# Kernel tuning notes

Measured on AMD Instinct MI355X. Metric: run time of the kernel, lower is better.

## Reference

```python
import jax, jax.numpy as jnp
import numpy as np

EMBED_DIM = 768
NUM_HEADS = 12


def setup_inputs() -> dict:
    key = jax.random.key(0)
    ks = jax.random.split(key, 9)
    B, N, C = 16, 1024, EMBED_DIM
    std = 1.0 / np.sqrt(C)
    x = jax.random.normal(ks[0], (B, N, C), dtype=jnp.float32)
    def w(k):
        return jax.random.normal(k, (C, C), dtype=jnp.float32) * std
    def b(k):
        return jax.random.normal(k, (C,), dtype=jnp.float32) * 0.01
    return {
        "x": x,
        "Wq": w(ks[1]), "bq": b(ks[2]),
        "Wk": w(ks[3]), "bk": b(ks[4]),
        "Wv": w(ks[5]), "bv": b(ks[6]),
        "Wo": w(ks[7]), "bo": b(ks[8]),
    }


def reference(x, Wq, bq, Wk, bk, Wv, bv, Wo, bo):
    B, N, C = x.shape
    H = NUM_HEADS
    Dh = C // H
    scale = 1.0 / np.sqrt(Dh)

    q = x @ Wq + bq  # (B, N, C)
    k = x @ Wk + bk
    v = x @ Wv + bv

    # Faithful to the original: (B, N, H, Dh) -> reshape(B*H, N, Dh)
    # WITHOUT transposing, exactly as torch_mla_core does (row-major reshape).
    q2 = q.reshape(B * H, N, Dh)
    k2 = k.reshape(B * H, N, Dh)
    v2 = v.reshape(B * H, N, Dh)

    scores = jnp.einsum('gld,gmd->glm', q2, k2) * scale  # (B*H, N, N)
    attn = jax.nn.softmax(scores, axis=-1)
    ctx2 = jnp.einsum('glm,gmd->gld', attn, v2)  # (B*H, N, Dh)

    ctx = ctx2.reshape(B, H, N, Dh).transpose(0, 2, 1, 3).reshape(B, N, C)
    out = ctx @ Wo + bo
    return out
```

## Files before the change

kernel.cpp:

```cpp
#include <hip/hip_runtime.h>
#include <cstdint>
#include <cstddef>

typedef unsigned short u16;
typedef __attribute__((ext_vector_type(8))) short s8v;
typedef __attribute__((ext_vector_type(4))) float f4v;
typedef __attribute__((ext_vector_type(8))) u16 u16x8;

#define AS1 __attribute__((address_space(1)))
#define AS3 __attribute__((address_space(3)))

#define BATCH 16
#define SEQ   1024
#define EMBED 768
#define HEADS 12
#define DH    64
#define GROUPS (BATCH*HEADS)
#define MTOT  (BATCH*SEQ)

__device__ __forceinline__ u16 f2bf(float f) {
    union { float f; uint32_t u; } v; v.f = f;
    uint32_t r = v.u + 0x7fffu + ((v.u >> 16) & 1u);
    return (u16)(r >> 16);
}

__device__ __forceinline__ void gll16(const u16* g, u16* l) {
    __builtin_amdgcn_global_load_lds((AS1 void*)g, (AS3 void*)l, 16, 0, 0);
}

__global__ void k_pack_x(const float* __restrict__ x, u16* __restrict__ xb, int n) {
    int i = (blockIdx.x * 256 + threadIdx.x) * 4;
    if (i + 3 < n) {
        float4 f = *(const float4*)(x + i);
        ushort4 o;
        o.x = f2bf(f.x); o.y = f2bf(f.y); o.z = f2bf(f.z); o.w = f2bf(f.w);
        *(ushort4*)(xb + i) = o;
    }
}

__global__ void k_pack_w(const float* __restrict__ Wq, const float* __restrict__ Wk,
                         const float* __restrict__ Wv, const float* __restrict__ Wo,
                         const float* __restrict__ bq, const float* __restrict__ bk,
                         const float* __restrict__ bv,
                         u16* __restrict__ wqkvT, u16* __restrict__ woT,
                         float* __restrict__ bqkv)
{
    const int NQKV = 2304 * 768;
    const int NO = 768 * 768;
    int t = blockIdx.x * 256 + threadIdx.x;
    if (t < NQKV) {
        int n = t % 2304, k = t / 2304;
        const float* src; int nn; float sc;
        if (n < 768)       { src = Wq; nn = n;        sc = 0.125f; }
        else if (n < 1536) { src = Wk; nn = n - 768;  sc = 1.0f;   }
        else               { src = Wv; nn = n - 1536; sc = 1.0f;   }
        wqkvT[(size_t)n * 768 + k] = f2bf(src[(size_t)k * 768 + nn] * sc);
    } else if (t < NQKV + NO) {
        int t2 = t - NQKV;
        int n = t2 % 768, k = t2 / 768;
        woT[(size_t)n * 768 + k] = f2bf(Wo[(size_t)k * 768 + n]);
    } else if (t < NQKV + NO + 2304) {
        int t3 = t - NQKV - NO;
        bqkv[t3] = (t3 < 768) ? bq[t3] * 0.125f
                 : ((t3 < 1536) ? bk[t3 - 768] : bv[t3 - 1536]);
    }
}

template<int MODE>
__global__ __launch_bounds__(256) void k_gemm(
    const u16* __restrict__ A, const u16* __restrict__ BT,
    const float* __restrict__ bias,
    u16* __restrict__ oq, u16* __restrict__ okk, u16* __restrict__ ov,
    float* __restrict__ of)
{
    __shared__ __attribute__((aligned(16))) u16 As[128 * 32];
    __shared__ __attribute__((aligned(16))) u16 Bs[128 * 32];
    const int tid = threadIdx.x;
    const int m0 = blockIdx.x * 128;
    const int n0 = blockIdx.y * 128;
    const int wv = tid >> 6;
    const int ln = tid & 63;
    const int l15 = ln & 15, quad = ln >> 4;
    const int wm = (wv >> 1) * 64, wn = (wv & 1) * 64;
    const int r = tid >> 2, c8 = (tid & 3) * 8;

    const u16* gA0 = A + (size_t)(m0 + r) * 768 + c8;
    const u16* gA1 = gA0 + 64 * 768;
    const u16* gB0 = BT + (size_t)(n0 + r) * 768 + c8;
    const u16* gB1 = gB0 + 64 * 768;
    u16* lA0 = As + wv * 512;
    u16* lA1 = As + 2048 + wv * 512;
    u16* lB0 = Bs + wv * 512;
    u16* lB1 = Bs + 2048 + wv * 512;

    f4v acc[4][4] = {};

    for (int kt = 0; kt < 24; ++kt) {
        const int ko = kt * 32;
        gll16(gA0 + ko, lA0);
        gll16(gA1 + ko, lA1);
        gll16(gB0 + ko, lB0);
        gll16(gB1 + ko, lB1);
        __syncthreads();
        s8v aF[4], bF[4];
#pragma unroll
        for (int i = 0; i < 4; ++i)
            aF[i] = *(const s8v*)(As + (wm + i * 16 + l15) * 32 + quad * 8);
#pragma unroll
        for (int j = 0; j < 4; ++j)
            bF[j] = *(const s8v*)(Bs + (wn + j * 16 + l15) * 32 + quad * 8);
#pragma unroll
        for (int i = 0; i < 4; ++i)
#pragma unroll
            for (int j = 0; j < 4; ++j)
                acc[i][j] = __builtin_amdgcn_mfma_f32_16x16x32_bf16(aF[i], bF[j], acc[i][j], 0, 0, 0);
        __syncthreads();
    }

#pragma unroll
    for (int j = 0; j < 4; ++j) {
        int n = n0 + wn + j * 16 + l15;
        float bs = bias[n];
        if (MODE == 0) {
            u16* dst; int nn;
            if (n < 768)       { dst = oq;  nn = n; }
            else if (n < 1536) { dst = okk; nn = n - 768; }
            else               { dst = ov;  nn = n - 1536; }
#pragma unroll
            for (int i = 0; i < 4; ++i) {
                int mrow = m0 + wm + i * 16 + quad * 4;
#pragma unroll
                for (int rg = 0; rg < 4; ++rg)
                    dst[(size_t)(mrow + rg) * 768 + nn] = f2bf(acc[i][j][rg] + bs);
            }
        } else {
#pragma unroll
            for (int i = 0; i < 4; ++i) {
                int mrow = m0 + wm + i * 16 + quad * 4;
#pragma unroll
                for (int rg = 0; rg < 4; ++rg)
                    of[(size_t)(mrow + rg) * 768 + n] = acc[i][j][rg] + bs;
            }
        }
    }
}

__global__ void k_transpose_v(const u16* __restrict__ v, u16* __restrict__ vt) {
    __shared__ __attribute__((aligned(16))) u16 ts[64 * 72];
    int g = blockIdx.x >> 4;
    int l0 = (blockIdx.x & 15) << 6;
    const u16* vg = v + (size_t)g * 65536;
    u16* vtg = vt + (size_t)g * 65536;
    int tid = threadIdx.x;
#pragma unroll
    for (int c = tid; c < 512; c += 256) {
        int l = c >> 3, d0 = (c & 7) * 8;
        *(uint4*)(ts + l * 72 + d0) = *(const uint4*)(vg + (size_t)(l0 + l) * 64 + d0);
    }
    __syncthreads();
#pragma unroll
    for (int c = tid; c < 512; c += 256) {
        int d = c >> 3, lc = (c & 7) * 8;
        u16x8 tv;
#pragma unroll
        for (int i = 0; i < 8; ++i) tv[i] = ts[(lc + i) * 72 + d];
        *(u16x8*)(vtg + (size_t)d * 1024 + l0 + lc) = tv;
    }
}

#define PS_OFF(q_, c_) ( ((q_) << 7) + ((((((c_) >> 3) ^ ((((q_) >> 2) & 3) << 1)) & 15) << 3) | ((c_) & 7)) )
#define KS_OFF(r_, c_) ( ((r_) >> 3) * 544 + ((r_) & 7) * 64 + (c_) )

__global__ __launch_bounds__(256) void k_attn(
    const u16* __restrict__ qb, const u16* __restrict__ kb,
    const u16* __restrict__ vt, u16* __restrict__ ctx)
{
    __shared__ __attribute__((aligned(16))) u16 Ks[16 * 544];
    __shared__ __attribute__((aligned(16))) u16 Vts[64 * 136];
    __shared__ __attribute__((aligned(16))) u16 U[64 * 128];

    const int g = blockIdx.x >> 4;
    const int q0 = (blockIdx.x & 15) << 6;
    const int tid = threadIdx.x, wv = tid >> 6;
    const int ln = tid & 63, l15 = ln & 15, quad = ln >> 4;
    const u16* qg = qb + (size_t)g * 65536;
    const u16* kg = kb + (size_t)g * 65536;
    const u16* vtg = vt + (size_t)g * 65536;

#pragma unroll
    for (int c = tid; c < 512; c += 256) {
        int r = c >> 3, d0 = (c & 7) * 8;
        *(uint4*)(U + r * 72 + d0) = *(const uint4*)(qg + (size_t)(q0 + r) * 64 + d0);
    }
    __syncthreads();
    s8v aQ0 = *(const s8v*)(U + (wv * 16 + l15) * 72 + quad * 8);
    s8v aQ1 = *(const s8v*)(U + (wv * 16 + l15) * 72 + 32 + quad * 8);

    f4v o[4] = {};
    float rsum[4] = {0.f, 0.f, 0.f, 0.f};

    for (int jt = 0; jt < 8; ++jt) {
        const int n0 = jt * 128;
        __syncthreads();

#pragma unroll
        for (int i = 0; i < 4; ++i) {
            int g8 = wv * 4 + i;
            gll16(kg + (size_t)(n0 + g8 * 8) * 64 + ln * 8, Ks + g8 * 544);
        }
#pragma unroll
        for (int c = tid; c < 1024; c += 256) {
            int d = c >> 4, c0 = (c & 15) * 8;
            *(uint4*)(Vts + d * 136 + c0) = *(const uint4*)(vtg + (size_t)d * 1024 + n0 + c0);
        }
        __syncthreads();

        f4v s[8];
#pragma unroll
        for (int ns = 0; ns < 8; ++ns) {
            int rK = ns * 16 + l15;
            s8v b0 = *(const s8v*)(Ks + KS_OFF(rK, quad * 8));
            s8v b1 = *(const s8v*)(Ks + KS_OFF(rK, quad * 8 + 32));
            f4v t = {};
            t = __builtin_amdgcn_mfma_f32_16x16x32_bf16(aQ0, b0, t, 0, 0, 0);
            t = __builtin_amdgcn_mfma_f32_16x16x32_bf16(aQ1, b1, t, 0, 0, 0);
            s[ns] = t;
        }

#pragma unroll
        for (int ns = 0; ns < 8; ++ns)
#pragma unroll
            for (int rg = 0; rg < 4; ++rg) {
                float p = __expf(s[ns][rg]);
                s[ns][rg] = p;
                rsum[rg] += p;
            }

#pragma unroll
        for (int ns = 0; ns < 8; ++ns)
#pragma unroll
            for (int rg = 0; rg < 4; ++rg) {
                int q = wv * 16 + quad * 4 + rg;
                U[PS_OFF(q, ns * 16 + l15)] = f2bf(s[ns][rg]);
            }

#pragma unroll
        for (int ks = 0; ks < 4; ++ks) {
            int m = wv * 16 + l15;
            int blk = ks * 4 + quad;
            int sw = ((l15 >> 2) & 3) << 1;
            s8v aP = *(const s8v*)(U + (m << 7) + (((blk ^ sw) & 15) << 3));
#pragma unroll
            for (int ds = 0; ds < 4; ++ds) {
                s8v bV = *(const s8v*)(Vts + (ds * 16 + l15) * 136 + ks * 32 + quad * 8);
                o[ds] = __builtin_amdgcn_mfma_f32_16x16x32_bf16(aP, bV, o[ds], 0, 0, 0);
            }
        }
    }

#pragma unroll
    for (int rg = 0; rg < 4; ++rg) {
        float v = rsum[rg];
        v += __shfl_xor(v, 1, 64);
        v += __shfl_xor(v, 2, 64);
        v += __shfl_xor(v, 4, 64);
        v += __shfl_xor(v, 8, 64);
        rsum[rg] = v;
    }

    const int b = g / 12, h = g % 12;
    u16* cbase = ctx + (size_t)b * 1024 * 768 + h * 64;
#pragma unroll
    for (int rg = 0; rg < 4; ++rg) {
        float inv = 1.0f / rsum[rg];
        int row = q0 + wv * 16 + quad * 4 + rg;
#pragma unroll
        for (int ds = 0; ds < 4; ++ds)
            cbase[(size_t)row * 768 + ds * 16 + l15] = f2bf(o[ds][rg] * inv);
    }
}

extern "C" void kernel_launch(void* const* d_in, const int* in_sizes, int n_in,
                              void* d_out, int out_size, void* d_ws, size_t ws_size,
                              hipStream_t stream) {
    const float* x  = (const float*)d_in[0];
    const float* Wq = (const float*)d_in[1];
    const float* bq = (const float*)d_in[2];
    const float* Wk = (const float*)d_in[3];
    const float* bk = (const float*)d_in[4];
    const float* Wv = (const float*)d_in[5];
    const float* bv = (const float*)d_in[6];
    const float* Wo = (const float*)d_in[7];
    const float* bo = (const float*)d_in[8];
    float* out = (float*)d_out;

    const size_t NTOK = (size_t)MTOT * EMBED;
    char* w = (char*)d_ws;
    u16* xb    = (u16*)w;              w += NTOK * 2;
    u16* qb    = (u16*)w;              w += NTOK * 2;
    u16* kb    = (u16*)w;              w += NTOK * 2;
    u16* vb    = (u16*)w;              w += NTOK * 2;
    u16* vtb   = (u16*)w;              w += NTOK * 2;
    u16* wqkvT = (u16*)w;              w += (size_t)2304 * 768 * 2;
    u16* woT   = (u16*)w;              w += (size_t)768 * 768 * 2;
    float* bqkv = (float*)w;           w += 2304 * 4;
    u16* ctx = xb;

    k_pack_x<<<12288, 256, 0, stream>>>(x, xb, (int)NTOK);
    k_pack_w<<<9225, 256, 0, stream>>>(Wq, Wk, Wv, Wo, bq, bk, bv, wqkvT, woT, bqkv);

    dim3 g1(128, 18);
    k_gemm<0><<<g1, 256, 0, stream>>>(xb, wqkvT, bqkv, qb, kb, vb, nullptr);

    k_transpose_v<<<3072, 256, 0, stream>>>(vb, vtb);
    k_attn<<<3072, 256, 0, stream>>>(qb, kb, vtb, ctx);

    dim3 g2(128, 6);
    k_gemm<1><<<g2, 256, 0, stream>>>(ctx, woT, bo, nullptr, nullptr, nullptr, out);
}
```

Measured before the change: 368.5 us.

## Merge pack kernels, XOR-swizzle K tile in LDS, repad V transpose buffer

Fuses the x and weight packing kernels into one launch to save a kernel launch and let the two jobs overlap. In attention, the K tile is now loaded with ordinary vector loads into an XOR-swizzled 128x64 LDS layout instead of global_load_lds into a padded layout, aiming to cut bank conflicts on the MFMA operand reads. The V transpose LDS row pitch changes from 72 to 80. The cost is that K loads now pass through registers rather than going directly to LDS.

```diff
diff --git a/kernel.cpp b/kernel.cpp
--- a/kernel.cpp
+++ b/kernel.cpp
@@ -1,4 +1,5 @@
 #include <hip/hip_runtime.h>
+#include <hip/hip_bf16.h>
 #include <cstdint>
 #include <cstddef>
 
@@ -15,7 +16,6 @@
 #define EMBED 768
 #define HEADS 12
 #define DH    64
-#define GROUPS (BATCH*HEADS)
 #define MTOT  (BATCH*SEQ)
 
 __device__ __forceinline__ u16 f2bf(float f) {
@@ -28,26 +28,28 @@
     __builtin_amdgcn_global_load_lds((AS1 void*)g, (AS3 void*)l, 16, 0, 0);
 }
 
-__global__ void k_pack_x(const float* __restrict__ x, u16* __restrict__ xb, int n) {
-    int i = (blockIdx.x * 256 + threadIdx.x) * 4;
-    if (i + 3 < n) {
-        float4 f = *(const float4*)(x + i);
-        ushort4 o;
-        o.x = f2bf(f.x); o.y = f2bf(f.y); o.z = f2bf(f.z); o.w = f2bf(f.w);
-        *(ushort4*)(xb + i) = o;
-    }
-}
-
-__global__ void k_pack_w(const float* __restrict__ Wq, const float* __restrict__ Wk,
-                         const float* __restrict__ Wv, const float* __restrict__ Wo,
-                         const float* __restrict__ bq, const float* __restrict__ bk,
-                         const float* __restrict__ bv,
-                         u16* __restrict__ wqkvT, u16* __restrict__ woT,
-                         float* __restrict__ bqkv)
+#define XBLOCKS 12288
+__global__ void k_pack(const float* __restrict__ x, u16* __restrict__ xb, int nx,
+                       const float* __restrict__ Wq, const float* __restrict__ Wk,
+                       const float* __restrict__ Wv, const float* __restrict__ Wo,
+                       const float* __restrict__ bq, const float* __restrict__ bk,
+                       const float* __restrict__ bv,
+                       u16* __restrict__ wqkvT, u16* __restrict__ woT,
+                       float* __restrict__ bqkv)
 {
+    if (blockIdx.x < XBLOCKS) {
+        int i = (blockIdx.x * 256 + threadIdx.x) * 4;
+        if (i + 3 < nx) {
+            float4 f = *(const float4*)(x + i);
+            ushort4 o;
+            o.x = f2bf(f.x); o.y = f2bf(f.y); o.z = f2bf(f.z); o.w = f2bf(f.w);
+            *(ushort4*)(xb + i) = o;
+        }
+        return;
+    }
     const int NQKV = 2304 * 768;
     const int NO = 768 * 768;
-    int t = blockIdx.x * 256 + threadIdx.x;
+    int t = (blockIdx.x - XBLOCKS) * 256 + threadIdx.x;
     if (t < NQKV) {
         int n = t % 2304, k = t / 2304;
         const float* src; int nn; float sc;
@@ -146,7 +148,7 @@
 }
 
 __global__ void k_transpose_v(const u16* __restrict__ v, u16* __restrict__ vt) {
-    __shared__ __attribute__((aligned(16))) u16 ts[64 * 72];
+    __shared__ __attribute__((aligned(16))) u16 ts[64 * 80];
     int g = blockIdx.x >> 4;
     int l0 = (blockIdx.x & 15) << 6;
     const u16* vg = v + (size_t)g * 65536;
@@ -155,7 +157,7 @@
 #pragma unroll
     for (int c = tid; c < 512; c += 256) {
         int l = c >> 3, d0 = (c & 7) * 8;
-        *(uint4*)(ts + l * 72 + d0) = *(const uint4*)(vg + (size_t)(l0 + l) * 64 + d0);
+        *(uint4*)(ts + l * 80 + d0) = *(const uint4*)(vg + (size_t)(l0 + l) * 64 + d0);
     }
     __syncthreads();
 #pragma unroll
@@ -163,19 +165,19 @@
         int d = c >> 3, lc = (c & 7) * 8;
         u16x8 tv;
 #pragma unroll
-        for (int i = 0; i < 8; ++i) tv[i] = ts[(lc + i) * 72 + d];
+        for (int i = 0; i < 8; ++i) tv[i] = ts[(lc + i) * 80 + d];
         *(u16x8*)(vtg + (size_t)d * 1024 + l0 + lc) = tv;
     }
 }
 
+#define KS2(r_, c_) ( ((r_) << 6) + (((((c_) >> 3) ^ ((r_) & 7)) & 7) << 3) + ((c_) & 7) )
 #define PS_OFF(q_, c_) ( ((q_) << 7) + ((((((c_) >> 3) ^ ((((q_) >> 2) & 3) << 1)) & 15) << 3) | ((c_) & 7)) )
-#define KS_OFF(r_, c_) ( ((r_) >> 3) * 544 + ((r_) & 7) * 64 + (c_) )
 
 __global__ __launch_bounds__(256) void k_attn(
     const u16* __restrict__ qb, const u16* __restrict__ kb,
     const u16* __restrict__ vt, u16* __restrict__ ctx)
 {
-    __shared__ __attribute__((aligned(16))) u16 Ks[16 * 544];
+    __shared__ __attribute__((aligned(16))) u16 Ks[128 * 64];
     __shared__ __attribute__((aligned(16))) u16 Vts[64 * 136];
     __shared__ __attribute__((aligned(16))) u16 U[64 * 128];
 
@@ -189,8 +191,8 @@
 
 #pragma unroll
     for (int c = tid; c < 512; c += 256) {
-        int r = c >> 3, d0 = (c & 7) * 8;
-        *(uint4*)(U + r * 72 + d0) = *(const uint4*)(qg + (size_t)(q0 + r) * 64 + d0);
+        int rr = c >> 3, d0 = (c & 7) * 8;
+        *(uint4*)(U + rr * 72 + d0) = *(const uint4*)(qg + (size_t)(q0 + rr) * 64 + d0);
     }
     __syncthreads();
     s8v aQ0 = *(const s8v*)(U + (wv * 16 + l15) * 72 + quad * 8);
@@ -205,8 +207,9 @@
 
 #pragma unroll
         for (int i = 0; i < 4; ++i) {
-            int g8 = wv * 4 + i;
-            gll16(kg + (size_t)(n0 + g8 * 8) * 64 + ln * 8, Ks + g8 * 544);
+            int t = tid + i * 256;
+            int rr = t >> 3, cb = (t & 7) << 3;
+            *(uint4*)(Ks + KS2(rr, cb)) = *(const uint4*)(kg + (size_t)(n0 + rr) * 64 + cb);
         }
 #pragma unroll
         for (int c = tid; c < 1024; c += 256) {
@@ -219,8 +222,8 @@
 #pragma unroll
         for (int ns = 0; ns < 8; ++ns) {
             int rK = ns * 16 + l15;
-            s8v b0 = *(const s8v*)(Ks + KS_OFF(rK, quad * 8));
-            s8v b1 = *(const s8v*)(Ks + KS_OFF(rK, quad * 8 + 32));
+            s8v b0 = *(const s8v*)(Ks + KS2(rK, quad * 8));
+            s8v b1 = *(const s8v*)(Ks + KS2(rK, quad * 8 + 32));
             f4v t = {};
             t = __builtin_amdgcn_mfma_f32_16x16x32_bf16(aQ0, b0, t, 0, 0, 0);
             t = __builtin_amdgcn_mfma_f32_16x16x32_bf16(aQ1, b1, t, 0, 0, 0);
@@ -269,7 +272,7 @@
     }
 
     const int b = g / 12, h = g % 12;
-    u16* cbase = ctx + (size_t)b * 1024 * 768 + h * 64;
+    u16* cbase = ctx + (size_t)b * 786432 + h * 64;
 #pragma unroll
     for (int rg = 0; rg < 4; ++rg) {
         float inv = 1.0f / rsum[rg];
@@ -306,8 +309,8 @@
     float* bqkv = (float*)w;           w += 2304 * 4;
     u16* ctx = xb;
 
-    k_pack_x<<<12288, 256, 0, stream>>>(x, xb, (int)NTOK);
-    k_pack_w<<<9225, 256, 0, stream>>>(Wq, Wk, Wv, Wo, bq, bk, bv, wqkvT, woT, bqkv);
+    k_pack<<<XBLOCKS + 9225, 256, 0, stream>>>(x, xb, (int)NTOK,
+        Wq, Wk, Wv, Wo, bq, bk, bv, wqkvT, woT, bqkv);
 
     dim3 g1(128, 18);
     k_gemm<0><<<g1, 256, 0, stream>>>(xb, wqkvT, bqkv, qb, kb, vb, nullptr);
```

Result: no change. 366.2 us (-0.6%).
